# Kernel optimization log

Measured on AMD Instinct MI355X. Metric: run time of the kernel, lower is better.

Reference implementation:

```python
import jax, jax.numpy as jnp
import numpy as np

K, D, P, C = 96, 256, 40, 8  # trials, embed dim, phoneme bins, gate hidden

def setup_inputs() -> dict:
    key = jax.random.key(0)
    ks = jax.random.split(key, 5)
    return {
        "enroll": jax.random.normal(ks[0], (K, D, P), jnp.float32),
        "test": jax.random.normal(ks[1], (K, D, P), jnp.float32),
        "fc1_w": jax.random.normal(ks[2], (C, 1), jnp.float32) * 0.5,
        "fc1_b": jax.random.normal(ks[3], (C,), jnp.float32) * 0.1,
        "fc2_w": jax.random.normal(ks[4], (1, C), jnp.float32) * 0.5,
    }

def _l2norm(x, axis):
    # torch F.normalize(p=2): x / max(||x||, eps)
    n = jnp.sqrt(jnp.sum(x * x, axis=axis, keepdims=True))
    return x / jnp.maximum(n, 1e-12)

def _gate(x, fc1_w, fc1_b, fc2_w):
    # tiny 1->C->1 MLP: fc2(tanh(fc1(x))), applied elementwise on x
    h = jnp.tanh(x[..., None] * fc1_w[:, 0] + fc1_b)   # [..., C]
    return jnp.einsum('...c,c->...', h, fc2_w[0])

def reference(enroll, test, fc1_w, fc1_b, fc2_w):
    e = _l2norm(enroll, axis=1)                        # [K, D, P]
    t = _l2norm(test, axis=1)                          # [K, D, P]
    # pho_matrix[k,l,i,j] = <e[k,:,i], t[l,:,j]>
    pho = jnp.einsum('kdi,ldj->klij', e, t)            # [K, K, P, P]
    cnt1 = jnp.sum(pho != 0, axis=-1).astype(pho.dtype) + 1e-6
    pho = _gate(pho, fc1_w, fc1_b, fc2_w) * pho        # gated elementwise
    pho = jnp.sum(pho, axis=-1) / cnt1                 # [K, K, P]
    cnt2 = jnp.sum(pho != 0, axis=-1).astype(pho.dtype) + 1e-6
    pho = _gate(pho, fc1_w, fc1_b, fc2_w) * pho        # [K, K, P]
    return jnp.sum(pho, axis=-1) / cnt2                # [K, K]
```

## Files before the change

kernel.cpp:

```cpp
#include <hip/hip_runtime.h>
#include <math.h>

#define KTR 96
#define DIM 256
#define PB  40
#define CH  8
#define MDIM 3840
#define ROWH 640
#define BM 160
#define BNS 128
#define BNV 120
#define LDA 40
#define SZA (BM * LDA * 2)
#define SZB (BNS * LDA * 2)
#define NTAB 2113

typedef _Float16 v8h __attribute__((ext_vector_type(8)));
typedef float    v4f __attribute__((ext_vector_type(4)));

#define CP16(g, l) __builtin_amdgcn_global_load_lds(                  \
    (const __attribute__((address_space(1))) void*)(g),               \
    (__attribute__((address_space(3))) void*)(l), 16, 0, 0)

__device__ __forceinline__ float gate_ref(float x, const float* w, const float* b, const float* v) {
    float g = 0.f;
    #pragma unroll
    for (int c = 0; c < CH; ++c) g = fmaf(v[c], tanhf(fmaf(w[c], x, b[c])), g);
    return g;
}

__global__ __launch_bounds__(256) void k_norm(const float* __restrict__ enroll,
                                              const float* __restrict__ test,
                                              const float* __restrict__ fc1_w,
                                              const float* __restrict__ fc1_b,
                                              const float* __restrict__ fc2_w,
                                              _Float16* __restrict__ XT,
                                              _Float16* __restrict__ XE,
                                              float2* __restrict__ gtabG) {
    int b = blockIdx.x, tid = threadIdx.x;

    if (b >= 2 * KTR) {
        int i = (b - 2 * KTR) * 256 + tid;
        if (i < NTAB) {
            float w[CH], bb[CH], vv[CH];
            #pragma unroll
            for (int c = 0; c < CH; ++c) { w[c] = fc1_w[c]; bb[c] = fc1_b[c]; vv[c] = fc2_w[c]; }
            float x0 = (float)(i - 1056) * 0.0009765625f;
            float g0 = gate_ref(x0, w, bb, vv);
            float g1 = gate_ref(x0 + 0.0009765625f, w, bb, vv);
            gtabG[i] = make_float2(g0, g1 - g0);
        }
        return;
    }

    bool isE = (b < KTR);
    int k = isE ? b : b - KTR;
    const float* src = (isE ? enroll : test) + (size_t)k * DIM * PB;

    __shared__ float S[DIM * 41];
    __shared__ float part[6 * PB];
    __shared__ float rn[PB];

    for (int i = tid; i < DIM * PB / 4; i += 256) {
        float4 v = ((const float4*)src)[i];
        int d = i / 10, c = i - d * 10;
        float* p = &S[d * 41 + c * 4];
        p[0] = v.x; p[1] = v.y; p[2] = v.z; p[3] = v.w;
    }
    __syncthreads();
    if (tid < 240) {
        int g = tid / PB, p = tid - (tid / PB) * PB;
        float acc = 0.f;
        for (int d = g; d < DIM; d += 6) {
            float x = S[d * 41 + p];
            acc = fmaf(x, x, acc);
        }
        part[g * PB + p] = acc;
    }
    __syncthreads();
    if (tid < PB) {
        float s = 0.f;
        #pragma unroll
        for (int g = 0; g < 6; ++g) s += part[g * PB + tid];
        rn[tid] = 1.0f / fmaxf(sqrtf(s), 1e-12f);
    }
    __syncthreads();

    _Float16* dst = isE ? XE : XT;
    #pragma unroll
    for (int i = 0; i < 5; ++i) {
        int idx = tid + i * 256;
        int p = idx >> 5, dg = idx & 31;
        int d0 = dg * 8;
        float r = rn[p];
        union { _Float16 f[8]; uint4 u; } hv, lv;
        #pragma unroll
        for (int j = 0; j < 8; ++j) {
            float x = S[(d0 + j) * 41 + p] * r;
            _Float16 h = (_Float16)x;
            hv.f[j] = h;
            lv.f[j] = (_Float16)((x - (float)h) * 4096.0f);
        }
        int kc = dg >> 2, dd = (dg & 3) * 8;
        size_t base = (size_t)(k * PB + p) * ROWH;
        if (isE) {
            *(uint4*)(dst + base + kc * 40 + dd)       = lv.u;
            *(uint4*)(dst + base + (8 + kc) * 40 + dd) = hv.u;
        } else {
            *(uint4*)(dst + base + kc * 40 + dd)       = hv.u;
            *(uint4*)(dst + base + (8 + kc) * 40 + dd) = lv.u;
        }
    }
}

struct Jobs {
    const char* gA[4]; int lA[4]; bool aA[4];
    const char* gB[3]; int lB[3]; bool aB[3];
};

__device__ __forceinline__ void issue(const Jobs& J, int it, int buf, void* LAp, void* LBp) {
    int kA = (it < 16) ? it : it - 16;
    int kB = (it < 16) ? it : it - 8;
    char* la = (char*)LAp + buf * SZA;
    char* lb = (char*)LBp + buf * SZB;
    #pragma unroll
    for (int j = 0; j < 4; ++j) if (J.aA[j]) CP16(J.gA[j] + kA * 80, la + J.lA[j]);
    #pragma unroll
    for (int j = 0; j < 3; ++j) if (J.aB[j]) CP16(J.gB[j] + kB * 80, lb + J.lB[j]);
}

__global__ __launch_bounds__(256, 3) void k_gemm(const _Float16* __restrict__ XT,
                                                 const _Float16* __restrict__ XE,
                                                 const float2* __restrict__ gtab,
                                                 const float* __restrict__ fc1_w,
                                                 const float* __restrict__ fc1_b,
                                                 const float* __restrict__ fc2_w,
                                                 float* __restrict__ out) {
    __shared__ __align__(16) _Float16 LA[2][BM * LDA];
    __shared__ __align__(16) _Float16 LB[2][BNS * LDA];
    __shared__ float ph2[4][132];

    int tid = threadIdx.x, lane = tid & 63, wv = tid >> 6;
    int m0 = blockIdx.y * BM;
    int n0 = blockIdx.x * BNV;

    Jobs J;
    #pragma unroll
    for (int j = 0; j < 4; ++j) {
        int idx = tid + j * 256;
        J.aA[j] = idx < BM * 5;
        int row = idx / 5, c5 = idx - row * 5;
        J.gA[j] = (const char*)XT + (size_t)(m0 + (J.aA[j] ? row : 0)) * (ROWH * 2) + c5 * 16;
        J.lA[j] = idx * 16;
    }
    #pragma unroll
    for (int j = 0; j < 3; ++j) {
        int idx = tid + j * 256;
        J.aB[j] = idx < BNS * 5;
        int row = idx / 5, c5 = idx - row * 5;
        int gr = n0 + row; if (gr > MDIM - 1) gr = MDIM - 1;
        J.gB[j] = (const char*)XE + (size_t)(J.aB[j] ? gr : 0) * (ROWH * 2) + c5 * 16;
        J.lB[j] = idx * 16;
    }

    int wm = (wv & 1) * 80;
    int wn = (wv >> 1) * 64;
    int r15 = lane & 15, q4 = lane >> 4;

    int aoff[5], boff[4];
    #pragma unroll
    for (int mt = 0; mt < 5; ++mt) aoff[mt] = (wm + mt * 16 + r15) * LDA + q4 * 8;
    #pragma unroll
    for (int nt = 0; nt < 4; ++nt) boff[nt] = (wn + nt * 16 + r15) * LDA + q4 * 8;

    v4f acc[5][4];
    #pragma unroll
    for (int mt = 0; mt < 5; ++mt)
        #pragma unroll
        for (int nt = 0; nt < 4; ++nt)
            acc[mt][nt] = (v4f)0.f;

    issue(J, 0, 0, LA, LB);
    for (int it = 0; it < 24; ++it) {
        int buf = it & 1;
        __syncthreads();
        if (it < 23) issue(J, it + 1, buf ^ 1, LA, LB);

        if (it == 16) {
            #pragma unroll
            for (int mt = 0; mt < 5; ++mt)
                #pragma unroll
                for (int nt = 0; nt < 4; ++nt)
                    acc[mt][nt] *= 0.000244140625f;
        }

        const _Float16* A = LA[buf];
        const _Float16* B = LB[buf];
        v8h af[5], bf[4];
        #pragma unroll
        for (int mt = 0; mt < 5; ++mt) af[mt] = *(const v8h*)(A + aoff[mt]);
        #pragma unroll
        for (int nt = 0; nt < 4; ++nt) bf[nt] = *(const v8h*)(B + boff[nt]);
        #pragma unroll
        for (int mt = 0; mt < 5; ++mt)
            #pragma unroll
            for (int nt = 0; nt < 4; ++nt)
                acc[mt][nt] = __builtin_amdgcn_mfma_f32_16x16x32_f16(af[mt], bf[nt], acc[mt][nt], 0, 0, 0);
    }

    const float inv40 = 1.0f / (40.0f + 1e-6f);
    int lgb = wm / 40;
    #pragma unroll
    for (int nt = 0; nt < 4; ++nt) {
        float s0 = 0.f, s1 = 0.f, t2 = 0.f;
        #pragma unroll
        for (int mt = 0; mt < 5; ++mt) {
            #pragma unroll
            for (int r = 0; r < 4; ++r) {
                float x = acc[mt][nt][r];
                float u = fmaf(x, 1024.0f, 1056.0f);
                int i = (int)u;
                i = min(max(i, 0), NTAB - 2);
                float f = u - (float)i;
                float2 tv = gtab[i];
                float xg = fmaf(f, tv.y, tv.x) * x;
                if (mt < 2)       s0 += xg;
                else if (mt == 2) t2 += xg;
                else              s1 += xg;
            }
        }
        bool lo = (q4 < 2);
        s0 += lo ? t2 : 0.f;
        s1 += lo ? 0.f : t2;
        s0 += __shfl_xor(s0, 16); s0 += __shfl_xor(s0, 32);
        s1 += __shfl_xor(s1, 16); s1 += __shfl_xor(s1, 32);
        if (q4 == 0) {
            int col = wn + nt * 16 + r15;
            ph2[lgb][col]     = s0 * inv40;
            ph2[lgb + 1][col] = s1 * inv40;
        }
    }
    __syncthreads();

    float w2[CH], b2[CH], v2[CH];
    #pragma unroll
    for (int c = 0; c < CH; ++c) { w2[c] = fc1_w[c]; b2[c] = fc1_b[c]; v2[c] = fc2_w[c]; }

    #pragma unroll
    for (int r = 0; r < 3; ++r) {
        float x = (lane < PB) ? ph2[wv][r * PB + lane] : 0.f;
        float s = gate_ref(x, w2, b2, v2) * x;
        #pragma unroll
        for (int off = 32; off; off >>= 1) s += __shfl_xor(s, off);
        if (lane == 0)
            out[(size_t)(blockIdx.x * 3 + r) * KTR + blockIdx.y * 4 + wv] = s * inv40;
    }
}

extern "C" void kernel_launch(void* const* d_in, const int* in_sizes, int n_in,
                              void* d_out, int out_size, void* d_ws, size_t ws_size,
                              hipStream_t stream) {
    const float* enroll = (const float*)d_in[0];
    const float* test   = (const float*)d_in[1];
    const float* fc1_w  = (const float*)d_in[2];
    const float* fc1_b  = (const float*)d_in[3];
    const float* fc2_w  = (const float*)d_in[4];
    float* out = (float*)d_out;

    _Float16* XT = (_Float16*)d_ws;
    _Float16* XE = XT + (size_t)MDIM * ROWH;
    float2* gtabG = (float2*)(XE + (size_t)MDIM * ROWH);

    k_norm<<<2 * KTR + 9, 256, 0, stream>>>(enroll, test, fc1_w, fc1_b, fc2_w, XT, XE, gtabG);
    dim3 g2(MDIM / BNV, MDIM / BM);
    k_gemm<<<g2, 256, 0, stream>>>(XT, XE, gtabG, fc1_w, fc1_b, fc2_w, out);
}
```

Measured before the change: 123.7 us.

## Replace async LDS double-buffer with register-staged loads and K=64 tiles

Drops the padded 40-half row layout and the direct global-to-LDS async copies, storing rows as plain 512-half arrays. The GEMM now loads each 64-wide K chunk into registers, writes it to a single padded LDS buffer (stride 72), and prefetches the next chunk into registers while the MFMAs run. This halves the main-loop iteration count and removes the per-copy predicates, at the cost of an extra barrier per iteration, higher register pressure and no LDS double buffering.

```diff
diff --git a/kernel.cpp b/kernel.cpp
--- a/kernel.cpp
+++ b/kernel.cpp
@@ -6,21 +6,15 @@
 #define PB  40
 #define CH  8
 #define MDIM 3840
-#define ROWH 640
+#define KK  512
 #define BM 160
 #define BNS 128
 #define BNV 120
-#define LDA 40
-#define SZA (BM * LDA * 2)
-#define SZB (BNS * LDA * 2)
+#define LDR 72
 #define NTAB 2113
 
 typedef _Float16 v8h __attribute__((ext_vector_type(8)));
 typedef float    v4f __attribute__((ext_vector_type(4)));
-
-#define CP16(g, l) __builtin_amdgcn_global_load_lds(                  \
-    (const __attribute__((address_space(1))) void*)(g),               \
-    (__attribute__((address_space(3))) void*)(l), 16, 0, 0)
 
 __device__ __forceinline__ float gate_ref(float x, const float* w, const float* b, const float* v) {
     float g = 0.f;
@@ -101,32 +95,15 @@
             hv.f[j] = h;
             lv.f[j] = (_Float16)((x - (float)h) * 4096.0f);
         }
-        int kc = dg >> 2, dd = (dg & 3) * 8;
-        size_t base = (size_t)(k * PB + p) * ROWH;
+        size_t base = (size_t)(k * PB + p) * KK;
         if (isE) {
-            *(uint4*)(dst + base + kc * 40 + dd)       = lv.u;
-            *(uint4*)(dst + base + (8 + kc) * 40 + dd) = hv.u;
+            *(uint4*)(dst + base + d0)       = lv.u;
+            *(uint4*)(dst + base + 256 + d0) = hv.u;
         } else {
-            *(uint4*)(dst + base + kc * 40 + dd)       = hv.u;
-            *(uint4*)(dst + base + (8 + kc) * 40 + dd) = lv.u;
-        }
-    }
-}
-
-struct Jobs {
-    const char* gA[4]; int lA[4]; bool aA[4];
-    const char* gB[3]; int lB[3]; bool aB[3];
-};
-
-__device__ __forceinline__ void issue(const Jobs& J, int it, int buf, void* LAp, void* LBp) {
-    int kA = (it < 16) ? it : it - 16;
-    int kB = (it < 16) ? it : it - 8;
-    char* la = (char*)LAp + buf * SZA;
-    char* lb = (char*)LBp + buf * SZB;
-    #pragma unroll
-    for (int j = 0; j < 4; ++j) if (J.aA[j]) CP16(J.gA[j] + kA * 80, la + J.lA[j]);
-    #pragma unroll
-    for (int j = 0; j < 3; ++j) if (J.aB[j]) CP16(J.gB[j] + kB * 80, lb + J.lB[j]);
+            *(uint4*)(dst + base + d0)       = hv.u;
+            *(uint4*)(dst + base + 256 + d0) = lv.u;
+        }
+    }
 }
 
 __global__ __launch_bounds__(256, 3) void k_gemm(const _Float16* __restrict__ XT,
@@ -136,31 +113,30 @@
                                                  const float* __restrict__ fc1_b,
                                                  const float* __restrict__ fc2_w,
                                                  float* __restrict__ out) {
-    __shared__ __align__(16) _Float16 LA[2][BM * LDA];
-    __shared__ __align__(16) _Float16 LB[2][BNS * LDA];
+    __shared__ __align__(16) _Float16 LA[BM * LDR];
+    __shared__ __align__(16) _Float16 LB[BNS * LDR];
     __shared__ float ph2[4][132];
 
     int tid = threadIdx.x, lane = tid & 63, wv = tid >> 6;
     int m0 = blockIdx.y * BM;
     int n0 = blockIdx.x * BNV;
 
-    Jobs J;
+    const uint4* gA[5]; int lAo[5];
+    #pragma unroll
+    for (int j = 0; j < 5; ++j) {
+        int idx = tid + j * 256;
+        int r = idx >> 3, c = idx & 7;
+        gA[j]  = (const uint4*)(XT + (size_t)(m0 + r) * KK) + c;
+        lAo[j] = r * LDR + c * 8;
+    }
+    const uint4* gB[4]; int lBo[4];
     #pragma unroll
     for (int j = 0; j < 4; ++j) {
         int idx = tid + j * 256;
-        J.aA[j] = idx < BM * 5;
-        int row = idx / 5, c5 = idx - row * 5;
-        J.gA[j] = (const char*)XT + (size_t)(m0 + (J.aA[j] ? row : 0)) * (ROWH * 2) + c5 * 16;
-        J.lA[j] = idx * 16;
-    }
-    #pragma unroll
-    for (int j = 0; j < 3; ++j) {
-        int idx = tid + j * 256;
-        J.aB[j] = idx < BNS * 5;
-        int row = idx / 5, c5 = idx - row * 5;
-        int gr = n0 + row; if (gr > MDIM - 1) gr = MDIM - 1;
-        J.gB[j] = (const char*)XE + (size_t)(J.aB[j] ? gr : 0) * (ROWH * 2) + c5 * 16;
-        J.lB[j] = idx * 16;
+        int r = idx >> 3, c = idx & 7;
+        int gr = n0 + r; if (gr > MDIM - 1) gr = MDIM - 1;
+        gB[j]  = (const uint4*)(XE + (size_t)gr * KK) + c;
+        lBo[j] = r * LDR + c * 8;
     }
 
     int wm = (wv & 1) * 80;
@@ -169,9 +145,9 @@
 
     int aoff[5], boff[4];
     #pragma unroll
-    for (int mt = 0; mt < 5; ++mt) aoff[mt] = (wm + mt * 16 + r15) * LDA + q4 * 8;
-    #pragma unroll
-    for (int nt = 0; nt < 4; ++nt) boff[nt] = (wn + nt * 16 + r15) * LDA + q4 * 8;
+    for (int mt = 0; mt < 5; ++mt) aoff[mt] = (wm + mt * 16 + r15) * LDR + q4 * 8;
+    #pragma unroll
+    for (int nt = 0; nt < 4; ++nt) boff[nt] = (wn + nt * 16 + r15) * LDR + q4 * 8;
 
     v4f acc[5][4];
     #pragma unroll
@@ -180,13 +156,26 @@
         for (int nt = 0; nt < 4; ++nt)
             acc[mt][nt] = (v4f)0.f;
 
-    issue(J, 0, 0, LA, LB);
-    for (int it = 0; it < 24; ++it) {
-        int buf = it & 1;
+    uint4 sa[5], sb[4];
+    #define GLOAD(IT) {                                                      \
+        int ka = ((IT) < 8) ? (IT) * 8 : ((IT) - 8) * 8;                     \
+        int kb = ((IT) < 8) ? (IT) * 8 : 32 + ((IT) - 8) * 8;                \
+        _Pragma("unroll")                                                    \
+        for (int j = 0; j < 5; ++j) sa[j] = gA[j][ka];                       \
+        _Pragma("unroll")                                                    \
+        for (int j = 0; j < 4; ++j) sb[j] = gB[j][kb]; }
+
+    GLOAD(0);
+    for (int it = 0; it < 12; ++it) {
         __syncthreads();
-        if (it < 23) issue(J, it + 1, buf ^ 1, LA, LB);
-
-        if (it == 16) {
+        #pragma unroll
+        for (int j = 0; j < 5; ++j) *(uint4*)(LA + lAo[j]) = sa[j];
+        #pragma unroll
+        for (int j = 0; j < 4; ++j) *(uint4*)(LB + lBo[j]) = sb[j];
+        __syncthreads();
+        if (it < 11) GLOAD(it + 1);
+
+        if (it == 8) {
             #pragma unroll
             for (int mt = 0; mt < 5; ++mt)
                 #pragma unroll
@@ -194,19 +183,21 @@
                     acc[mt][nt] *= 0.000244140625f;
         }
 
-        const _Float16* A = LA[buf];
-        const _Float16* B = LB[buf];
-        v8h af[5], bf[4];
-        #pragma unroll
-        for (int mt = 0; mt < 5; ++mt) af[mt] = *(const v8h*)(A + aoff[mt]);
-        #pragma unroll
-        for (int nt = 0; nt < 4; ++nt) bf[nt] = *(const v8h*)(B + boff[nt]);
-        #pragma unroll
-        for (int mt = 0; mt < 5; ++mt)
-            #pragma unroll
-            for (int nt = 0; nt < 4; ++nt)
-                acc[mt][nt] = __builtin_amdgcn_mfma_f32_16x16x32_f16(af[mt], bf[nt], acc[mt][nt], 0, 0, 0);
-    }
+        #pragma unroll
+        for (int h = 0; h < 2; ++h) {
+            v8h af[5], bf[4];
+            #pragma unroll
+            for (int mt = 0; mt < 5; ++mt) af[mt] = *(const v8h*)(LA + aoff[mt] + h * 32);
+            #pragma unroll
+            for (int nt = 0; nt < 4; ++nt) bf[nt] = *(const v8h*)(LB + boff[nt] + h * 32);
+            #pragma unroll
+            for (int mt = 0; mt < 5; ++mt)
+                #pragma unroll
+                for (int nt = 0; nt < 4; ++nt)
+                    acc[mt][nt] = __builtin_amdgcn_mfma_f32_16x16x32_f16(af[mt], bf[nt], acc[mt][nt], 0, 0, 0);
+        }
+    }
+    #undef GLOAD
 
     const float inv40 = 1.0f / (40.0f + 1e-6f);
     int lgb = wm / 40;
@@ -268,8 +259,8 @@
     float* out = (float*)d_out;
 
     _Float16* XT = (_Float16*)d_ws;
-    _Float16* XE = XT + (size_t)MDIM * ROWH;
-    float2* gtabG = (float2*)(XE + (size_t)MDIM * ROWH);
+    _Float16* XE = XT + (size_t)MDIM * KK;
+    float2* gtabG = (float2*)(XE + (size_t)MDIM * KK);
 
     k_norm<<<2 * KTR + 9, 256, 0, stream>>>(enroll, test, fc1_w, fc1_b, fc2_w, XT, XE, gtabG);
     dim3 g2(MDIM / BNV, MDIM / BM);
```

Measured after the change: 185.8 us. +50.1%, slower.
